# Kernel tuning notes

Hardware: AMD Instinct MI355X
Metric: run time of the kernel (lower is better)

The kernel has to match this reference:

```python
import jax, jax.numpy as jnp
import numpy as np

B, L, HSIZE = 16, 512, 1024
H, D = 16, 64  # HHEAD = HSIZE/base, HBASE = 64

def setup_inputs() -> dict:
    key = jax.random.key(0)
    ks = jax.random.split(key, 10)
    inp = {
        'v': jax.random.normal(ks[0], (B, L, HSIZE), jnp.float32),
        'k': jax.random.normal(ks[1], (B, L, HSIZE), jnp.float32),
        'q': jax.random.normal(ks[2], (B, L, HSIZE), jnp.float32),
        'img_abs': jax.random.normal(ks[3], (B, L, HSIZE), jnp.float32),
        'Wv': jax.random.normal(ks[4], (HSIZE, HSIZE), jnp.float32) * 0.02,
        'Wk': jax.random.normal(ks[5], (HSIZE, HSIZE), jnp.float32) * 0.02,
        'Wq': jax.random.normal(ks[6], (HSIZE, HSIZE), jnp.float32) * 0.02,
        'Wm': jax.random.normal(ks[7], (HSIZE, HSIZE), jnp.float32) * 0.02,
        'abs_mask': jax.random.bernoulli(ks[8], 0.1, (B, 1, L, L)),
        'mask': jax.random.bernoulli(ks[9], 0.1, (B, 1, L, L)),
    }
    return inp

def reference(v, k, q, img_abs, Wv, Wk, Wq, Wm, abs_mask, mask):
    nb = q.shape[0]
    # Linear (no bias) then split heads: [B, L, HSIZE] -> [B, H, L, D]
    def heads(x):
        return x.reshape(nb, -1, H, D).transpose(0, 2, 1, 3)
    vh = heads(v @ Wv.T)
    kh = heads(k @ Wk.T)
    qh = heads(q @ Wq.T)
    ph = heads(img_abs)
    scale = 1.0 / jnp.sqrt(jnp.asarray(D, qh.dtype))
    # modulate: attention of q over positional features, residual-added to q
    s1 = jnp.einsum('bhqd,bhpd->bhqp', qh, ph) * scale
    s1 = jnp.where(abs_mask, jnp.asarray(-1e9, s1.dtype), s1)
    qh = qh + jnp.einsum('bhqp,bhpd->bhqd', jax.nn.softmax(s1, axis=-1), ph)
    # main attention (dropout = identity in eval mode)
    s2 = jnp.einsum('bhqd,bhkd->bhqk', qh, kh) * scale
    s2 = jnp.where(mask, jnp.asarray(-1e9, s2.dtype), s2)
    atted = jnp.einsum('bhqk,bhkd->bhqd', jax.nn.softmax(s2, axis=-1), vh)
    atted = atted.transpose(0, 2, 1, 3).reshape(nb, -1, H * D)
    return atted @ Wm.T
```

## Files before the change

### kernel.cpp

```cpp
#include <hip/hip_runtime.h>

typedef unsigned short u16;
typedef unsigned int u32;
typedef unsigned long long u64;
typedef __attribute__((ext_vector_type(8))) short short8;
typedef __attribute__((ext_vector_type(4))) float f32x4;

#define NB 16
#define SL 512
#define HS 1024
#define NHEAD 16
#define HD 64

typedef const __attribute__((address_space(1))) u32* gas_t;
typedef __attribute__((address_space(3))) u32* las_t;

__device__ __forceinline__ void gld16(const u16* g, u16* l) {
  __builtin_amdgcn_global_load_lds((gas_t)g, (las_t)l, 16, 0, 0);
}

__device__ __forceinline__ u16 f2bf(float f) {
  union { float f; unsigned u; } c; c.f = f;
  unsigned r = c.u + 0x7FFFu + ((c.u >> 16) & 1u);
  return (u16)(r >> 16);
}
__device__ __forceinline__ float bf2f(u16 u) {
  union { float f; unsigned u; } c; c.u = ((unsigned)u) << 16;
  return c.f;
}

__global__ __launch_bounds__(256) void cvt_bf16(const float* __restrict__ in,
                                                u16* __restrict__ out, long n) {
  long i = ((long)blockIdx.x * 256 + threadIdx.x) * 4;
  if (i >= n) return;
  float4 f = *(const float4*)(in + i);
  uint2 u;
  u.x = (unsigned)f2bf(f.x) | ((unsigned)f2bf(f.y) << 16);
  u.y = (unsigned)f2bf(f.z) | ((unsigned)f2bf(f.w) << 16);
  *(uint2*)(out + i) = u;
}

__global__ __launch_bounds__(256) void cvt_w4(const float* __restrict__ a,
                                              const float* __restrict__ b,
                                              const float* __restrict__ c,
                                              const float* __restrict__ d,
                                              u16* __restrict__ o, long n) {
  const float* in = (blockIdx.y == 0) ? a : (blockIdx.y == 1) ? b
                     : (blockIdx.y == 2) ? c : d;
  u16* out = o + (long)blockIdx.y * n;
  long i = ((long)blockIdx.x * 256 + threadIdx.x) * 4;
  if (i >= n) return;
  float4 f = *(const float4*)(in + i);
  uint2 u;
  u.x = (unsigned)f2bf(f.x) | ((unsigned)f2bf(f.y) << 16);
  u.y = (unsigned)f2bf(f.z) | ((unsigned)f2bf(f.w) << 16);
  *(uint2*)(out + i) = u;
}

__global__ __launch_bounds__(256) void pack_mask(const int* __restrict__ m0,
                                                 const int* __restrict__ m1,
                                                 u64* __restrict__ o0,
                                                 u64* __restrict__ o1, long n) {
  long i = (long)blockIdx.x * 256 + threadIdx.x;
  const int* m = blockIdx.y ? m1 : m0;
  u64* o = blockIdx.y ? o1 : o0;
  u64 bits = __ballot(m[i] != 0);
  if ((threadIdx.x & 63) == 0) o[i >> 6] = bits;
}

template<bool CF32>
__global__ __launch_bounds__(256) void gemm_bt(const u16* __restrict__ A,
                                               const u16* __restrict__ W,
                                               void* __restrict__ C,
                                               int M, int N, int K) {
  __shared__ u16 As[128 * 64];
  __shared__ u16 Bs[128 * 64];
  const int tid = threadIdx.x;
  const int wave = tid >> 6, lane = tid & 63;
  const int quad = lane >> 4, l16 = lane & 15;
  const int l7 = l16 & 7;
  const int row0 = blockIdx.x * 128, col0 = blockIdx.y * 128;
  const int wm = (wave >> 1) * 64, wn = (wave & 1) * 64;
  const int lrow = lane >> 3;
  const int scb = (lane & 7) ^ lrow;

  f32x4 acc[4][4];
#pragma unroll
  for (int mt = 0; mt < 4; ++mt)
#pragma unroll
    for (int nt = 0; nt < 4; ++nt) acc[mt][nt] = (f32x4){0.f, 0.f, 0.f, 0.f};

  const u16* Ab = A + (long)row0 * K;
  const u16* Wb = W + (long)col0 * K;

  for (int k0 = 0; k0 < K; k0 += 64) {
    __syncthreads();
#pragma unroll
    for (int it = 0; it < 4; ++it) {
      int seg = wave * 4 + it;
      int r = seg * 8 + lrow;
      gld16(Ab + (long)r * K + k0 + scb * 8, As + seg * 512);
      gld16(Wb + (long)r * K + k0 + scb * 8, Bs + seg * 512);
    }
    __syncthreads();
#pragma unroll
    for (int kt = 0; kt < 2; ++kt) {
      short8 af[4], bw[4];
#pragma unroll
      for (int mt = 0; mt < 4; ++mt)
        af[mt] = *(const short8*)(As + (wm + mt * 16 + l16) * 64 +
                                  (((kt * 4 + quad) ^ l7) * 8));
#pragma unroll
      for (int nt = 0; nt < 4; ++nt)
        bw[nt] = *(const short8*)(Bs + (wn + nt * 16 + l16) * 64 +
                                  (((kt * 4 + quad) ^ l7) * 8));
#pragma unroll
      for (int mt = 0; mt < 4; ++mt)
#pragma unroll
        for (int nt = 0; nt < 4; ++nt)
          acc[mt][nt] = __builtin_amdgcn_mfma_f32_16x16x32_bf16(
              af[mt], bw[nt], acc[mt][nt], 0, 0, 0);
    }
  }
#pragma unroll
  for (int mt = 0; mt < 4; ++mt)
#pragma unroll
    for (int nt = 0; nt < 4; ++nt)
#pragma unroll
      for (int i = 0; i < 4; ++i) {
        long r = row0 + wm + mt * 16 + quad * 4 + i;
        long c = col0 + wn + nt * 16 + l16;
        float v = acc[mt][nt][i];
        if constexpr (CF32)
          ((float*)C)[r * N + c] = v;
        else
          ((u16*)C)[r * N + c] = f2bf(v);
      }
}

__global__ __launch_bounds__(256) void attn(const u16* __restrict__ Qp,
                                            const u16* __restrict__ Kp,
                                            const u16* __restrict__ Vp,
                                            const u32* __restrict__ Bits,
                                            u16* __restrict__ Op,
                                            int residual) {
  __shared__ u16 Qs[64][72];
  __shared__ u16 Ks[64][72];
  __shared__ u16 Vs[64][72];
  __shared__ u16 Ps[64][72];
  const int tid = threadIdx.x;
  const int wave = tid >> 6, lane = tid & 63;
  const int quad = lane >> 4, l16 = lane & 15;
  const int qt = blockIdx.x, h = blockIdx.y, b = blockIdx.z;
  const int q0 = qt * 64;
  const long bs = (long)SL * HS;
  const u16* Qb = Qp + (long)b * bs + h * HD;
  const u16* Kb = Kp + (long)b * bs + h * HD;
  const u16* Vb = Vp + (long)b * bs + h * HD;
  const u32* Mb = Bits + (long)b * SL * 16;

  const int sr = tid >> 2, sds = (tid & 3) * 16;
  {
    const uint4* s = (const uint4*)(Qb + (long)(q0 + sr) * HS + sds);
    *(uint4*)&Qs[sr][sds] = s[0];
    *(uint4*)&Qs[sr][sds + 8] = s[1];
  }

  float l_i[4] = {0.f, 0.f, 0.f, 0.f};
  f32x4 o[4];
#pragma unroll
  for (int nt = 0; nt < 4; ++nt) o[nt] = (f32x4){0.f, 0.f, 0.f, 0.f};

  const int vxor = ((sds >> 4) & 3) << 4;
  const int vcol = sr ^ vxor;

  for (int t = 0; t < 8; ++t) {
    const int k0 = t * 64;
    __syncthreads();
    {
      const uint4* sk = (const uint4*)(Kb + (long)(k0 + sr) * HS + sds);
      *(uint4*)&Ks[sr][sds] = sk[0];
      *(uint4*)&Ks[sr][sds + 8] = sk[1];
      uint4 v0 = *(const uint4*)(Vb + (long)(k0 + sr) * HS + sds);
      uint4 v1 = *(const uint4*)(Vb + (long)(k0 + sr) * HS + sds + 8);
      union { uint4 q[2]; u16 e[16]; } tv;
      tv.q[0] = v0; tv.q[1] = v1;
#pragma unroll
      for (int j = 0; j < 16; ++j) Vs[sds + j][vcol] = tv.e[j];
    }
    __syncthreads();
    f32x4 s[4];
#pragma unroll
    for (int nt = 0; nt < 4; ++nt) s[nt] = (f32x4){0.f, 0.f, 0.f, 0.f};
#pragma unroll
    for (int kt = 0; kt < 2; ++kt) {
      short8 aq = *(const short8*)&Qs[wave * 16 + l16][kt * 32 + quad * 8];
#pragma unroll
      for (int nt = 0; nt < 4; ++nt) {
        short8 bk = *(const short8*)&Ks[nt * 16 + l16][kt * 32 + quad * 8];
        s[nt] = __builtin_amdgcn_mfma_f32_16x16x32_bf16(aq, bk, s[nt], 0, 0, 0);
      }
    }
#pragma unroll
    for (int i = 0; i < 4; ++i) {
      int gr = q0 + wave * 16 + quad * 4 + i;
      uint2 mw = *(const uint2*)&Mb[(long)gr * 16 + t * 2];
#pragma unroll
      for (int nt = 0; nt < 4; ++nt) {
        u32 w = (nt & 2) ? mw.y : mw.x;
        int msk = (w >> ((nt & 1) * 16 + l16)) & 1;
        float p = msk ? 0.f : __expf(s[nt][i] * 0.125f);
        s[nt][i] = p;
        l_i[i] += p;
      }
    }
#pragma unroll
    for (int i = 0; i < 4; ++i) {
      int prow = wave * 16 + quad * 4 + i;
#pragma unroll
      for (int nt = 0; nt < 4; ++nt)
        Ps[prow][(nt * 16 + l16) ^ (quad << 3)] = f2bf(s[nt][i]);
    }
    __syncthreads();
#pragma unroll
    for (int kt = 0; kt < 2; ++kt) {
      short8 ap = *(const short8*)&Ps[wave * 16 + l16]
                                    [(kt * 32 + quad * 8) ^ ((l16 >> 2) << 3)];
#pragma unroll
      for (int nt = 0; nt < 4; ++nt) {
        short8 bv = *(const short8*)&Vs[nt * 16 + l16]
                                      [(kt * 32 + quad * 8) ^ ((nt & 3) << 4)];
        o[nt] = __builtin_amdgcn_mfma_f32_16x16x32_bf16(ap, bv, o[nt], 0, 0, 0);
      }
    }
  }
  u16* Ob = Op + (long)b * bs + h * HD;
#pragma unroll
  for (int i = 0; i < 4; ++i) {
    float rs = l_i[i];
#pragma unroll
    for (int off = 8; off >= 1; off >>= 1) rs += __shfl_xor(rs, off, 64);
    float inv = 1.f / rs;
    int r = q0 + wave * 16 + quad * 4 + i;
#pragma unroll
    for (int nt = 0; nt < 4; ++nt) {
      float val = o[nt][i] * inv;
      if (residual) val += bf2f(Qs[wave * 16 + quad * 4 + i][nt * 16 + l16]);
      Ob[(long)r * HS + nt * 16 + l16] = f2bf(val);
    }
  }
}

extern "C" void kernel_launch(void* const* d_in, const int* in_sizes, int n_in,
                              void* d_out, int out_size, void* d_ws,
                              size_t ws_size, hipStream_t stream) {
  const float* v   = (const float*)d_in[0];
  const float* k   = (const float*)d_in[1];
  const float* q   = (const float*)d_in[2];
  const float* img = (const float*)d_in[3];
  const float* Wv  = (const float*)d_in[4];
  const float* Wk  = (const float*)d_in[5];
  const float* Wq  = (const float*)d_in[6];
  const float* Wm  = (const float*)d_in[7];
  const int* absm  = (const int*)d_in[8];
  const int* mask  = (const int*)d_in[9];
  float* out = (float*)d_out;

  const long NTOK = (long)NB * SL * HS;
  const long NW   = (long)HS * HS;
  const long NM   = (long)NB * SL * SL;
  u16* ws  = (u16*)d_ws;
  u16* xb  = ws;
  u16* pb  = ws + 1 * NTOK;
  u16* vh  = ws + 2 * NTOK;
  u16* kh  = ws + 3 * NTOK;
  u16* qh  = ws + 4 * NTOK;
  u16* w4  = ws + 5 * NTOK;
  u64* bt0 = (u64*)(w4 + 4 * NW);
  u64* bt1 = bt0 + NM / 64;
  u16* qm  = xb;
  u16* att = qh;

  dim3 gg(NB * SL / 128, HS / 128);
  dim3 ga(SL / 64, NHEAD, NB);

  cvt_bf16<<<(unsigned)(NTOK / 1024), 256, 0, stream>>>(img, pb, NTOK);
  cvt_w4<<<dim3((unsigned)(NW / 1024), 4), 256, 0, stream>>>(Wv, Wk, Wq, Wm, w4, NW);
  pack_mask<<<dim3((unsigned)(NM / 256), 2), 256, 0, stream>>>(absm, mask, bt0, bt1, NM);

  cvt_bf16<<<(unsigned)(NTOK / 1024), 256, 0, stream>>>(v, xb, NTOK);
  gemm_bt<false><<<gg, 256, 0, stream>>>(xb, w4 + 0 * NW, vh, NB * SL, HS, HS);
  cvt_bf16<<<(unsigned)(NTOK / 1024), 256, 0, stream>>>(k, xb, NTOK);
  gemm_bt<false><<<gg, 256, 0, stream>>>(xb, w4 + 1 * NW, kh, NB * SL, HS, HS);
  cvt_bf16<<<(unsigned)(NTOK / 1024), 256, 0, stream>>>(q, xb, NTOK);
  gemm_bt<false><<<gg, 256, 0, stream>>>(xb, w4 + 2 * NW, qh, NB * SL, HS, HS);

  attn<<<ga, 256, 0, stream>>>(qh, pb, pb, (const u32*)bt0, qm, 1);
  attn<<<ga, 256, 0, stream>>>(qm, kh, vh, (const u32*)bt1, att, 0);

  gemm_bt<true><<<gg, 256, 0, stream>>>(att, w4 + 3 * NW, out, NB * SL, HS, HS);
}
```

Baseline: 418.2 us.

## Retile GEMM to 64x128 blocks and attention to 128 query rows with register-held Q

The projection GEMM switches to 64x128 output tiles, doubling the block count and setting an occupancy hint of 4 blocks per CU. The attention kernel processes 128 query rows per block, with each wave owning 32 rows. Q fragments now live in registers instead of shared memory, and K tiles are loaded with direct global-to-LDS copies into an XOR-swizzled layout. This is meant to amortize K/V tile loads over more queries and raise GEMM occupancy. The cost is half as many attention blocks (1024), more registers per thread, and an unswizzled P layout in LDS that may cause bank conflicts.

New measurement: 431.3 us. 1.03x slower.

```diff
diff --git a/kernel.cpp b/kernel.cpp
--- a/kernel.cpp
+++ b/kernel.cpp
@@ -69,24 +69,24 @@
 }
 
 template<bool CF32>
-__global__ __launch_bounds__(256) void gemm_bt(const u16* __restrict__ A,
-                                               const u16* __restrict__ W,
-                                               void* __restrict__ C,
-                                               int M, int N, int K) {
-  __shared__ u16 As[128 * 64];
+__global__ __launch_bounds__(256, 4) void gemm_bt(const u16* __restrict__ A,
+                                                  const u16* __restrict__ W,
+                                                  void* __restrict__ C,
+                                                  int M, int N, int K) {
+  __shared__ u16 As[64 * 64];
   __shared__ u16 Bs[128 * 64];
   const int tid = threadIdx.x;
   const int wave = tid >> 6, lane = tid & 63;
   const int quad = lane >> 4, l16 = lane & 15;
   const int l7 = l16 & 7;
-  const int row0 = blockIdx.x * 128, col0 = blockIdx.y * 128;
-  const int wm = (wave >> 1) * 64, wn = (wave & 1) * 64;
+  const int row0 = blockIdx.x * 64, col0 = blockIdx.y * 128;
+  const int wm = (wave >> 1) * 32, wn = (wave & 1) * 64;
   const int lrow = lane >> 3;
   const int scb = (lane & 7) ^ lrow;
 
-  f32x4 acc[4][4];
-#pragma unroll
-  for (int mt = 0; mt < 4; ++mt)
+  f32x4 acc[2][4];
+#pragma unroll
+  for (int mt = 0; mt < 2; ++mt)
 #pragma unroll
     for (int nt = 0; nt < 4; ++nt) acc[mt][nt] = (f32x4){0.f, 0.f, 0.f, 0.f};
 
@@ -96,18 +96,21 @@
   for (int k0 = 0; k0 < K; k0 += 64) {
     __syncthreads();
 #pragma unroll
+    for (int it = 0; it < 2; ++it) {
+      int seg = wave * 2 + it;
+      gld16(Ab + (long)(seg * 8 + lrow) * K + k0 + scb * 8, As + seg * 512);
+    }
+#pragma unroll
     for (int it = 0; it < 4; ++it) {
       int seg = wave * 4 + it;
-      int r = seg * 8 + lrow;
-      gld16(Ab + (long)r * K + k0 + scb * 8, As + seg * 512);
-      gld16(Wb + (long)r * K + k0 + scb * 8, Bs + seg * 512);
+      gld16(Wb + (long)(seg * 8 + lrow) * K + k0 + scb * 8, Bs + seg * 512);
     }
     __syncthreads();
 #pragma unroll
     for (int kt = 0; kt < 2; ++kt) {
-      short8 af[4], bw[4];
-#pragma unroll
-      for (int mt = 0; mt < 4; ++mt)
+      short8 af[2], bw[4];
+#pragma unroll
+      for (int mt = 0; mt < 2; ++mt)
         af[mt] = *(const short8*)(As + (wm + mt * 16 + l16) * 64 +
                                   (((kt * 4 + quad) ^ l7) * 8));
 #pragma unroll
@@ -115,7 +118,7 @@
         bw[nt] = *(const short8*)(Bs + (wn + nt * 16 + l16) * 64 +
                                   (((kt * 4 + quad) ^ l7) * 8));
 #pragma unroll
-      for (int mt = 0; mt < 4; ++mt)
+      for (int mt = 0; mt < 2; ++mt)
 #pragma unroll
         for (int nt = 0; nt < 4; ++nt)
           acc[mt][nt] = __builtin_amdgcn_mfma_f32_16x16x32_bf16(
@@ -123,7 +126,7 @@
     }
   }
 #pragma unroll
-  for (int mt = 0; mt < 4; ++mt)
+  for (int mt = 0; mt < 2; ++mt)
 #pragma unroll
     for (int nt = 0; nt < 4; ++nt)
 #pragma unroll
@@ -144,43 +147,54 @@
                                             const u32* __restrict__ Bits,
                                             u16* __restrict__ Op,
                                             int residual) {
-  __shared__ u16 Qs[64][72];
-  __shared__ u16 Ks[64][72];
+  __shared__ u16 Ks[64 * 64];
   __shared__ u16 Vs[64][72];
-  __shared__ u16 Ps[64][72];
+  __shared__ u16 Ps[128][72];
   const int tid = threadIdx.x;
   const int wave = tid >> 6, lane = tid & 63;
   const int quad = lane >> 4, l16 = lane & 15;
+  const int l7 = l16 & 7;
   const int qt = blockIdx.x, h = blockIdx.y, b = blockIdx.z;
-  const int q0 = qt * 64;
+  const int q0 = qt * 128;
   const long bs = (long)SL * HS;
   const u16* Qb = Qp + (long)b * bs + h * HD;
   const u16* Kb = Kp + (long)b * bs + h * HD;
   const u16* Vb = Vp + (long)b * bs + h * HD;
   const u32* Mb = Bits + (long)b * SL * 16;
+  const int lrow = lane >> 3;
+  const int scb = (lane & 7) ^ lrow;
+
+  short8 qf[2][2];
+#pragma unroll
+  for (int rf = 0; rf < 2; ++rf)
+#pragma unroll
+    for (int kt = 0; kt < 2; ++kt) {
+      int row = q0 + wave * 32 + rf * 16 + l16;
+      qf[rf][kt] = *(const short8*)(Qb + (long)row * HS + kt * 32 + quad * 8);
+    }
+
+  float l_i[2][4];
+  f32x4 o[2][4];
+#pragma unroll
+  for (int rf = 0; rf < 2; ++rf)
+#pragma unroll
+    for (int nt = 0; nt < 4; ++nt) {
+      o[rf][nt] = (f32x4){0.f, 0.f, 0.f, 0.f};
+      l_i[rf][nt] = 0.f;
+    }
 
   const int sr = tid >> 2, sds = (tid & 3) * 16;
-  {
-    const uint4* s = (const uint4*)(Qb + (long)(q0 + sr) * HS + sds);
-    *(uint4*)&Qs[sr][sds] = s[0];
-    *(uint4*)&Qs[sr][sds + 8] = s[1];
-  }
-
-  float l_i[4] = {0.f, 0.f, 0.f, 0.f};
-  f32x4 o[4];
-#pragma unroll
-  for (int nt = 0; nt < 4; ++nt) o[nt] = (f32x4){0.f, 0.f, 0.f, 0.f};
-
-  const int vxor = ((sds >> 4) & 3) << 4;
-  const int vcol = sr ^ vxor;
+  const int vcol = sr ^ (((sds >> 4) & 3) << 4);
 
   for (int t = 0; t < 8; ++t) {
     const int k0 = t * 64;
     __syncthreads();
+#pragma unroll
+    for (int it = 0; it < 2; ++it) {
+      int seg = wave * 2 + it;
+      gld16(Kb + (long)(k0 + seg * 8 + lrow) * HS + scb * 8, Ks + seg * 512);
+    }
     {
-      const uint4* sk = (const uint4*)(Kb + (long)(k0 + sr) * HS + sds);
-      *(uint4*)&Ks[sr][sds] = sk[0];
-      *(uint4*)&Ks[sr][sds + 8] = sk[1];
       uint4 v0 = *(const uint4*)(Vb + (long)(k0 + sr) * HS + sds);
       uint4 v1 = *(const uint4*)(Vb + (long)(k0 + sr) * HS + sds + 8);
       union { uint4 q[2]; u16 e[16]; } tv;
@@ -189,66 +203,73 @@
       for (int j = 0; j < 16; ++j) Vs[sds + j][vcol] = tv.e[j];
     }
     __syncthreads();
-    f32x4 s[4];
-#pragma unroll
-    for (int nt = 0; nt < 4; ++nt) s[nt] = (f32x4){0.f, 0.f, 0.f, 0.f};
+    f32x4 s[2][4];
+#pragma unroll
+    for (int rf = 0; rf < 2; ++rf)
+#pragma unroll
+      for (int nt = 0; nt < 4; ++nt) s[rf][nt] = (f32x4){0.f, 0.f, 0.f, 0.f};
+#pragma unroll
+    for (int kt = 0; kt < 2; ++kt)
+#pragma unroll
+      for (int nt = 0; nt < 4; ++nt) {
+        short8 bk = *(const short8*)(Ks + (nt * 16 + l16) * 64 +
+                                     (((kt * 4 + quad) ^ l7) * 8));
+#pragma unroll
+        for (int rf = 0; rf < 2; ++rf)
+          s[rf][nt] = __builtin_amdgcn_mfma_f32_16x16x32_bf16(qf[rf][kt], bk,
+                                                              s[rf][nt], 0, 0, 0);
+      }
+#pragma unroll
+    for (int rf = 0; rf < 2; ++rf)
+#pragma unroll
+      for (int i = 0; i < 4; ++i) {
+        int gr = q0 + wave * 32 + rf * 16 + quad * 4 + i;
+        uint2 mw = *(const uint2*)&Mb[(long)gr * 16 + t * 2];
+#pragma unroll
+        for (int nt = 0; nt < 4; ++nt) {
+          u32 w = (nt & 2) ? mw.y : mw.x;
+          int msk = (w >> ((nt & 1) * 16 + l16)) & 1;
+          float p = msk ? 0.f : __expf(s[rf][nt][i] * 0.125f);
+          l_i[rf][i] += p;
+          Ps[wave * 32 + rf * 16 + quad * 4 + i][nt * 16 + l16] = f2bf(p);
+        }
+      }
+    __syncthreads();
 #pragma unroll
     for (int kt = 0; kt < 2; ++kt) {
-      short8 aq = *(const short8*)&Qs[wave * 16 + l16][kt * 32 + quad * 8];
-#pragma unroll
-      for (int nt = 0; nt < 4; ++nt) {
-        short8 bk = *(const short8*)&Ks[nt * 16 + l16][kt * 32 + quad * 8];
-        s[nt] = __builtin_amdgcn_mfma_f32_16x16x32_bf16(aq, bk, s[nt], 0, 0, 0);
-      }
-    }
-#pragma unroll
-    for (int i = 0; i < 4; ++i) {
-      int gr = q0 + wave * 16 + quad * 4 + i;
-      uint2 mw = *(const uint2*)&Mb[(long)gr * 16 + t * 2];
-#pragma unroll
-      for (int nt = 0; nt < 4; ++nt) {
-        u32 w = (nt & 2) ? mw.y : mw.x;
-        int msk = (w >> ((nt & 1) * 16 + l16)) & 1;
-        float p = msk ? 0.f : __expf(s[nt][i] * 0.125f);
-        s[nt][i] = p;
-        l_i[i] += p;
-      }
-    }
-#pragma unroll
-    for (int i = 0; i < 4; ++i) {
-      int prow = wave * 16 + quad * 4 + i;
-#pragma unroll
-      for (int nt = 0; nt < 4; ++nt)
-        Ps[prow][(nt * 16 + l16) ^ (quad << 3)] = f2bf(s[nt][i]);
-    }
-    __syncthreads();
-#pragma unroll
-    for (int kt = 0; kt < 2; ++kt) {
-      short8 ap = *(const short8*)&Ps[wave * 16 + l16]
-                                    [(kt * 32 + quad * 8) ^ ((l16 >> 2) << 3)];
+      short8 ap[2];
+#pragma unroll
+      for (int rf = 0; rf < 2; ++rf)
+        ap[rf] = *(const short8*)&Ps[wave * 32 + rf * 16 + l16]
+                                    [kt * 32 + quad * 8];
 #pragma unroll
       for (int nt = 0; nt < 4; ++nt) {
         short8 bv = *(const short8*)&Vs[nt * 16 + l16]
                                       [(kt * 32 + quad * 8) ^ ((nt & 3) << 4)];
-        o[nt] = __builtin_amdgcn_mfma_f32_16x16x32_bf16(ap, bv, o[nt], 0, 0, 0);
+#pragma unroll
+        for (int rf = 0; rf < 2; ++rf)
+          o[rf][nt] = __builtin_amdgcn_mfma_f32_16x16x32_bf16(ap[rf], bv,
+                                                              o[rf][nt], 0, 0, 0);
       }
     }
   }
   u16* Ob = Op + (long)b * bs + h * HD;
 #pragma unroll
-  for (int i = 0; i < 4; ++i) {
-    float rs = l_i[i];
-#pragma unroll
-    for (int off = 8; off >= 1; off >>= 1) rs += __shfl_xor(rs, off, 64);
-    float inv = 1.f / rs;
-    int r = q0 + wave * 16 + quad * 4 + i;
-#pragma unroll
-    for (int nt = 0; nt < 4; ++nt) {
-      float val = o[nt][i] * inv;
-      if (residual) val += bf2f(Qs[wave * 16 + quad * 4 + i][nt * 16 + l16]);
-      Ob[(long)r * HS + nt * 16 + l16] = f2bf(val);
-    }
-  }
+  for (int rf = 0; rf < 2; ++rf)
+#pragma unroll
+    for (int i = 0; i < 4; ++i) {
+      float rs = l_i[rf][i];
+#pragma unroll
+      for (int off = 8; off >= 1; off >>= 1) rs += __shfl_xor(rs, off, 64);
+      float inv = 1.f / rs;
+      int r = q0 + wave * 32 + rf * 16 + quad * 4 + i;
+#pragma unroll
+      for (int nt = 0; nt < 4; ++nt) {
+        float val = o[rf][nt][i] * inv;
+        if (residual) val += bf2f(Qb[(long)r * HS + nt * 16 + l16]);
+        Ob[(long)r * HS + nt * 16 + l16] = f2bf(val);
+      }
+    }
 }
 
 extern "C" void kernel_launch(void* const* d_in, const int* in_sizes, int n_in,
@@ -281,8 +302,8 @@
   u16* qm  = xb;
   u16* att = qh;
 
-  dim3 gg(NB * SL / 128, HS / 128);
-  dim3 ga(SL / 64, NHEAD, NB);
+  dim3 gg(NB * SL / 64, HS / 128);
+  dim3 ga(SL / 128, NHEAD, NB);
 
   cvt_bf16<<<(unsigned)(NTOK / 1024), 256, 0, stream>>>(img, pb, NTOK);
   cvt_w4<<<dim3((unsigned)(NW / 1024), 4), 256, 0, stream>>>(Wv, Wk, Wq, Wm, w4, NW);
```
